# Kernel tuning notes

Hardware: AMD Instinct MI355X
Metric: run time of the kernel (lower is better)

Reference implementation:

```python
import jax, jax.numpy as jnp
import numpy as np

N_NODES = 100000
N_EDGES = 1600000
IN_DIM = 64
OUT_DIM = 64


def setup_inputs() -> dict:
    key = jax.random.key(0)
    k_x, k_e, k_wm, k_bm, k_wu, k_bu = jax.random.split(key, 6)
    x = jax.random.normal(k_x, (N_NODES, IN_DIM), dtype=jnp.float32)
    edge_index = jax.random.randint(k_e, (2, N_EDGES), 0, N_NODES, dtype=jnp.int64)
    # PyTorch Linear default init: U(-1/sqrt(fan_in), 1/sqrt(fan_in))
    lim_m = 1.0 / np.sqrt(2 * IN_DIM)
    lim_u = 1.0 / np.sqrt(IN_DIM + OUT_DIM)
    W_msg = jax.random.uniform(k_wm, (2 * IN_DIM, OUT_DIM), jnp.float32, -lim_m, lim_m)
    b_msg = jax.random.uniform(k_bm, (OUT_DIM,), jnp.float32, -lim_m, lim_m)
    W_upd = jax.random.uniform(k_wu, (IN_DIM + OUT_DIM, OUT_DIM), jnp.float32, -lim_u, lim_u)
    b_upd = jax.random.uniform(k_bu, (OUT_DIM,), jnp.float32, -lim_u, lim_u)
    return {"x": x, "edge_index": edge_index, "W_msg": W_msg, "b_msg": b_msg,
            "W_upd": W_upd, "b_upd": b_upd}


def reference(x, edge_index, W_msg, b_msg, W_upd, b_upd):
    num_nodes = x.shape[0]
    source, target = edge_index[0], edge_index[1]
    # gather endpoint features and compute messages: [E, 2*in] -> [E, out]
    edge_feats = jnp.concatenate([x[source], x[target]], axis=-1)
    messages = jax.nn.relu(edge_feats @ W_msg + b_msg)
    # mean aggregation onto target nodes
    agg_sum = jax.ops.segment_sum(messages, target, num_segments=num_nodes)
    counts = jax.ops.segment_sum(jnp.ones_like(target, dtype=x.dtype), target,
                                 num_segments=num_nodes)
    aggregated = agg_sum / jnp.clip(counts, 1.0, None)[:, None]
    # update MLP: [N, in+out] -> [N, out]
    updated = jax.nn.relu(jnp.concatenate([x, aggregated], axis=-1) @ W_upd + b_upd)
    return updated
```

## Files before the change

kernel.cpp:

```cpp
#include <hip/hip_runtime.h>
#include <hip/hip_bf16.h>

#define N_NODES 100000
#define N_EDGES 1600000
#define DIM 64
#define NB 196
#define CAP 9216
#define SMASK 0x1FFFFu
#define P1 391
#define T1 781
#define R1 (T1 * 64)
#define T2 196

typedef __attribute__((ext_vector_type(8))) short bf16x8;
typedef __attribute__((ext_vector_type(4))) float f32x4;
typedef __attribute__((ext_vector_type(2))) float f32x2;

__device__ __forceinline__ unsigned short f2bs(float f) {
    __hip_bfloat16 h = __float2bfloat16(f);
    return *reinterpret_cast<unsigned short*>(&h);
}

__device__ __forceinline__ void transform_tile(
    const float* __restrict__ x, const unsigned short* WB,
    const float* __restrict__ b_msg,
    unsigned int* __restrict__ Xs8, unsigned int* __restrict__ Xt8,
    int r0, int lane)
{
    f32x4 acc[8];
    #pragma unroll
    for (int ct = 0; ct < 8; ++ct) acc[ct] = (f32x4){0.f, 0.f, 0.f, 0.f};

    const int r = r0 + (lane & 15);
    #pragma unroll
    for (int kk = 0; kk < 2; ++kk) {
        const int off = kk * 32 + ((lane >> 4) << 3);
        const float4* xp = reinterpret_cast<const float4*>(&x[r * 64 + off]);
        const float4 p0 = xp[0], p1 = xp[1];
        bf16x8 a;
        a[0] = (short)f2bs(p0.x); a[1] = (short)f2bs(p0.y);
        a[2] = (short)f2bs(p0.z); a[3] = (short)f2bs(p0.w);
        a[4] = (short)f2bs(p1.x); a[5] = (short)f2bs(p1.y);
        a[6] = (short)f2bs(p1.z); a[7] = (short)f2bs(p1.w);
        #pragma unroll
        for (int ct = 0; ct < 8; ++ct) {
            const bf16x8 b = *reinterpret_cast<const bf16x8*>(
                &WB[(((ct << 1) | kk) * 64 + lane) << 3]);
            acc[ct] = __builtin_amdgcn_mfma_f32_16x16x32_bf16(a, b, acc[ct], 0, 0, 0);
        }
    }

    const int fr = lane & 15;
    const int rb = r0 + ((lane >> 4) << 2);
    const float bj0 = b_msg[fr],      bj1 = b_msg[16 + fr];
    const float bj2 = b_msg[32 + fr], bj3 = b_msg[48 + fr];
    #pragma unroll
    for (int q = 0; q < 4; ++q) {
        unsigned int xs = 0;
        xs = (unsigned)__builtin_amdgcn_cvt_pk_fp8_f32(acc[0][q], acc[1][q], (int)xs, false);
        xs = (unsigned)__builtin_amdgcn_cvt_pk_fp8_f32(acc[2][q], acc[3][q], (int)xs, true);
        Xs8[(rb + q) * 16 + fr] = xs;
        unsigned int xt = 0;
        xt = (unsigned)__builtin_amdgcn_cvt_pk_fp8_f32(acc[4][q] + bj0, acc[5][q] + bj1, (int)xt, false);
        xt = (unsigned)__builtin_amdgcn_cvt_pk_fp8_f32(acc[6][q] + bj2, acc[7][q] + bj3, (int)xt, true);
        Xt8[(rb + q) * 16 + fr] = xt;
    }
}

__global__ __launch_bounds__(256) void k1_part_xform(
    const float* __restrict__ x, const float* __restrict__ W_msg,
    const float* __restrict__ b_msg,
    unsigned int* __restrict__ Xs8, unsigned int* __restrict__ Xt8,
    const int* __restrict__ eidx, int* __restrict__ bcursor,
    unsigned int* __restrict__ pairs,
    const float* __restrict__ W_upd, unsigned short* __restrict__ wfrag)
{
    __shared__ __align__(16) char smem[35200];
    const int tid = threadIdx.x, lane = tid & 63, wid = tid >> 6;

    if (blockIdx.x >= P1 + T1) {
        for (int i = tid; i < 8192; i += 256) {
            const int j = i & 7, l = (i >> 3) & 63, kk = (i >> 9) & 3, ct = i >> 11;
            const int hi = l >> 4;
            int k;
            if (kk < 2) k = kk * 32 + (hi << 3) + j;
            else        k = 64 + ((j & 3) << 4) + ((kk - 2) << 3) + (hi << 1) + (j >> 2);
            const int c = ct * 16 + (l & 15);
            wfrag[i] = f2bs(W_upd[k * 64 + c]);
        }
    } else if (blockIdx.x >= P1) {
        unsigned short* WB = reinterpret_cast<unsigned short*>(smem);
        const int tb = blockIdx.x - P1;
        for (int i = tid; i < 8192; i += 256) {
            const int j = i & 7, l = (i >> 3) & 63, kk = (i >> 9) & 1, ct = i >> 10;
            const int k = kk * 32 + ((l >> 4) << 3) + j;
            const int c = ct * 16 + (l & 15);
            WB[i] = f2bs(W_msg[(((c >> 6) << 6) + k) * 64 + (c & 63)]);
        }
        __syncthreads();
        transform_tile(x, WB, b_msg, Xs8, Xt8, tb * 64 + wid * 16, lane);
    } else {
        unsigned int* sbuf = reinterpret_cast<unsigned int*>(smem);
        int* dbase = reinterpret_cast<int*>(smem + 16384);
        int* tcnt  = reinterpret_cast<int*>(smem + 32768);
        int* toff  = tcnt + NB;
        int* gpos  = toff + NB;
        int* wsum  = gpos + NB;

        const int base = blockIdx.x * 4096;
        const int tcount = min(4096, N_EDGES - base);
        if (tid < NB) tcnt[tid] = 0;
        __syncthreads();

        unsigned int pk[16]; int bb[16]; int rk[16];
        #pragma unroll
        for (int j = 0; j < 16; ++j) {
            const int idx = base + j * 256 + tid;
            bb[j] = -1;
            if (idx < N_EDGES) {
                const int sv = eidx[idx];
                const int tv = eidx[N_EDGES + idx];
                bb[j] = tv >> 9;
                pk[j] = (unsigned)sv | ((unsigned)(tv & 511) << 17);
                rk[j] = atomicAdd(&tcnt[bb[j]], 1);
            }
        }
        __syncthreads();

        const int v = (tid < NB) ? tcnt[tid] : 0;
        int s = v;
        #pragma unroll
        for (int d = 1; d < 64; d <<= 1) { int u = __shfl_up(s, d); if (lane >= d) s += u; }
        if (lane == 63) wsum[wid] = s;
        __syncthreads();
        if (wid == 0) {
            int ws = (lane < 4) ? wsum[lane] : 0;
            #pragma unroll
            for (int d = 1; d < 4; d <<= 1) { int u = __shfl_up(ws, d); if (lane >= d) ws += u; }
            if (lane < 4) wsum[lane] = ws;
        }
        __syncthreads();
        const int exc = (wid ? wsum[wid - 1] : 0) + s - v;
        if (tid < NB) {
            toff[tid] = exc;
            gpos[tid] = tid * CAP + (v ? atomicAdd(&bcursor[tid], v) : 0);
        }
        __syncthreads();

        #pragma unroll
        for (int j = 0; j < 16; ++j) {
            if (bb[j] >= 0) {
                const int l = toff[bb[j]] + rk[j];
                sbuf[l]  = pk[j];
                dbase[l] = gpos[bb[j]] + rk[j];
            }
        }
        __syncthreads();
        for (int i = tid; i < tcount; i += 256)
            pairs[dbase[i]] = sbuf[i];
    }
}

__global__ __launch_bounds__(1024) void k2_sort_xform(
    const int* __restrict__ bcursor, const unsigned int* __restrict__ pairs,
    int* __restrict__ csr, int* __restrict__ deg, int* __restrict__ row,
    const float* __restrict__ x, const float* __restrict__ W_msg,
    const float* __restrict__ b_msg,
    unsigned int* __restrict__ Xs8, unsigned int* __restrict__ Xt8)
{
    __shared__ __align__(16) char smem[59424];
    const int tid = threadIdx.x, lane = tid & 63, wid = tid >> 6;

    if (blockIdx.x >= NB) {
        unsigned short* WB = reinterpret_cast<unsigned short*>(smem);
        const int tb = blockIdx.x - NB;
        for (int i = tid; i < 8192; i += 1024) {
            const int j = i & 7, l = (i >> 3) & 63, kk = (i >> 9) & 1, ct = i >> 10;
            const int k = kk * 32 + ((l >> 4) << 3) + j;
            const int c = ct * 16 + (l & 15);
            WB[i] = f2bs(W_msg[(((c >> 6) << 6) + k) * 64 + (c & 63)]);
        }
        __syncthreads();
        const int r0 = R1 + tb * 256 + wid * 16;
        if (r0 >= N_NODES) return;
        transform_tile(x, WB, b_msg, Xs8, Xt8, r0, lane);
    } else {
        unsigned int*   ebuf = reinterpret_cast<unsigned int*>(smem);
        unsigned short* rbuf = reinterpret_cast<unsigned short*>(smem + 36864);
        int* ncnt = reinterpret_cast<int*>(smem + 55296);
        int* noff = reinterpret_cast<int*>(smem + 57344);
        int* wsum = reinterpret_cast<int*>(smem + 59392);

        const int b = blockIdx.x;
        const int s0 = b * CAP;
        const int cnt = bcursor[b];
        if (tid < 512) ncnt[tid] = 0;
        __syncthreads();

        for (int i = tid; i < cnt; i += 1024) {
            const unsigned int p = pairs[s0 + i];
            ebuf[i] = p;
            rbuf[i] = (unsigned short)atomicAdd(&ncnt[p >> 17], 1);
        }
        __syncthreads();

        int v = 0, s = 0;
        if (tid < 512) {
            v = ncnt[tid];
            s = v;
            #pragma unroll
            for (int d = 1; d < 64; d <<= 1) { int u = __shfl_up(s, d); if (lane >= d) s += u; }
            if (lane == 63) wsum[wid] = s;
        }
        __syncthreads();
        if (wid == 0) {
            int ws = (lane < 8) ? wsum[lane] : 0;
            #pragma unroll
            for (int d = 1; d < 8; d <<= 1) { int u = __shfl_up(ws, d); if (lane >= d) ws += u; }
            if (lane < 8) wsum[lane] = ws;
        }
        __syncthreads();
        if (tid < 512) {
            const int exc = (wid ? wsum[wid - 1] : 0) + s - v;
            noff[tid] = exc;
            const int n = b * 512 + tid;
            if (n < N_NODES) { deg[n] = v; row[n] = s0 + exc; }
        }
        __syncthreads();

        for (int i = tid; i < cnt; i += 1024) {
            const unsigned int p = ebuf[i];
            csr[s0 + noff[p >> 17] + (int)rbuf[i]] = (int)(p & SMASK);
        }
    }
}

__device__ __forceinline__ void acc_fp8(unsigned int u,
    float t0, float t1, float t2, float t3,
    float& a0, float& a1, float& a2, float& a3)
{
    const f32x2 lo = __builtin_amdgcn_cvt_pk_f32_fp8(u, false);
    const f32x2 hi = __builtin_amdgcn_cvt_pk_f32_fp8(u, true);
    a0 += fmaxf(lo.x + t0, 0.f);
    a1 += fmaxf(lo.y + t1, 0.f);
    a2 += fmaxf(hi.x + t2, 0.f);
    a3 += fmaxf(hi.y + t3, 0.f);
}

__global__ __launch_bounds__(1024, 8) void agg_update(
    const int* __restrict__ row, const int* __restrict__ deg,
    const int* __restrict__ csr,
    const unsigned int* __restrict__ Xs8, const unsigned int* __restrict__ Xt8,
    const float* __restrict__ x, const unsigned short* __restrict__ wfrag,
    const float* __restrict__ b_upd, float* __restrict__ out)
{
    __shared__ unsigned short WB[8192];
    __shared__ uint2 aggT[16][18];

    const int tid = threadIdx.x, lane = tid & 63, w = tid >> 6;
    const int n0 = blockIdx.x * 16;
    const int fr = lane & 15, hi = lane >> 4;

    float4 px0, px1, px2, px3; float bj = 0.f;
    if (w < 4) {
        const int r = n0 + fr;
        const float4* xp = reinterpret_cast<const float4*>(&x[r * 64 + (hi << 3)]);
        px0 = xp[0]; px1 = xp[1];
        const float4* xq = reinterpret_cast<const float4*>(&x[r * 64 + 32 + (hi << 3)]);
        px2 = xq[0]; px3 = xq[1];
        bj = b_upd[w * 16 + fr];
    }

    reinterpret_cast<bf16x8*>(WB)[tid] = reinterpret_cast<const bf16x8*>(wfrag)[tid];

    const int n = n0 + w;
    const int c = lane & 15, q = lane >> 4;
    const int start = row[n], d = deg[n];
    const unsigned int tp = Xt8[n * 16 + c];
    const f32x2 tlo = __builtin_amdgcn_cvt_pk_f32_fp8(tp, false);
    const f32x2 thi = __builtin_amdgcn_cvt_pk_f32_fp8(tp, true);
    const float t0 = tlo.x, t1 = tlo.y, t2 = thi.x, t3 = thi.y;
    float a0 = 0.f, a1 = 0.f, a2 = 0.f, a3 = 0.f;

    if (d > 0) {
        int i = 0;
        for (; i + 32 <= d; i += 32) {
            int sv[8];
            #pragma unroll
            for (int k = 0; k < 8; ++k) sv[k] = csr[start + i + 4 * k + q];
            unsigned int u[8];
            #pragma unroll
            for (int k = 0; k < 8; ++k) u[k] = Xs8[sv[k] * 16 + c];
            #pragma unroll
            for (int k = 0; k < 8; ++k) acc_fp8(u[k], t0, t1, t2, t3, a0, a1, a2, a3);
        }
        const int rem = d - i;
        if (rem > 0) {
            const int lastIdx = start + d - 1;
            int sv[8]; bool vm[8];
            #pragma unroll
            for (int k = 0; k < 8; ++k) {
                const int e = i + 4 * k + q;
                vm[k] = (e < d);
                sv[k] = csr[vm[k] ? (start + e) : lastIdx];
            }
            unsigned int u[8];
            #pragma unroll
            for (int k = 0; k < 8; ++k) u[k] = Xs8[sv[k] * 16 + c];
            #pragma unroll
            for (int k = 0; k < 8; ++k) {
                const f32x2 lo = __builtin_amdgcn_cvt_pk_f32_fp8(u[k], false);
                const f32x2 hi2 = __builtin_amdgcn_cvt_pk_f32_fp8(u[k], true);
                if (vm[k]) {
                    a0 += fmaxf(lo.x + t0, 0.f);
                    a1 += fmaxf(lo.y + t1, 0.f);
                    a2 += fmaxf(hi2.x + t2, 0.f);
                    a3 += fmaxf(hi2.y + t3, 0.f);
                }
            }
        }
    }

    a0 += __shfl_xor(a0, 16); a0 += __shfl_xor(a0, 32);
    a1 += __shfl_xor(a1, 16); a1 += __shfl_xor(a1, 32);
    a2 += __shfl_xor(a2, 16); a2 += __shfl_xor(a2, 32);
    a3 += __shfl_xor(a3, 16); a3 += __shfl_xor(a3, 32);
    if (q == 0) {
        const float inv = (d > 0) ? 1.0f / (float)d : 0.f;
        uint2 v2;
        v2.x = (unsigned)f2bs(a0 * inv) | ((unsigned)f2bs(a1 * inv) << 16);
        v2.y = (unsigned)f2bs(a2 * inv) | ((unsigned)f2bs(a3 * inv) << 16);
        aggT[w][c] = v2;
    }
    __syncthreads();

    if (w < 4) {
        const int ct = w;
        f32x4 acc = (f32x4){0.f, 0.f, 0.f, 0.f};
        #pragma unroll
        for (int kk = 0; kk < 4; ++kk) {
            bf16x8 a;
            if (kk == 0) {
                a[0] = (short)f2bs(px0.x); a[1] = (short)f2bs(px0.y);
                a[2] = (short)f2bs(px0.z); a[3] = (short)f2bs(px0.w);
                a[4] = (short)f2bs(px1.x); a[5] = (short)f2bs(px1.y);
                a[6] = (short)f2bs(px1.z); a[7] = (short)f2bs(px1.w);
            } else if (kk == 1) {
                a[0] = (short)f2bs(px2.x); a[1] = (short)f2bs(px2.y);
                a[2] = (short)f2bs(px2.z); a[3] = (short)f2bs(px2.w);
                a[4] = (short)f2bs(px3.x); a[5] = (short)f2bs(px3.y);
                a[6] = (short)f2bs(px3.z); a[7] = (short)f2bs(px3.w);
            } else {
                a = *reinterpret_cast<const bf16x8*>(
                    &aggT[fr][((kk - 2) << 3) + (hi << 1)]);
            }
            const bf16x8 b = *reinterpret_cast<const bf16x8*>(
                &WB[(((ct << 2) | kk) * 64 + lane) << 3]);
            acc = __builtin_amdgcn_mfma_f32_16x16x32_bf16(a, b, acc, 0, 0, 0);
        }
        const int rb = n0 + (hi << 2);
        const int cc = ct * 16 + fr;
        #pragma unroll
        for (int qq = 0; qq < 4; ++qq)
            out[(rb + qq) * 64 + cc] = fmaxf(acc[qq] + bj, 0.f);
    }
}

extern "C" void kernel_launch(void* const* d_in, const int* in_sizes, int n_in,
                              void* d_out, int out_size, void* d_ws, size_t ws_size,
                              hipStream_t stream) {
    const float* x     = (const float*)d_in[0];
    const int*   eidx  = (const int*)  d_in[1];
    const float* W_msg = (const float*)d_in[2];
    const float* b_msg = (const float*)d_in[3];
    const float* W_upd = (const float*)d_in[4];
    const float* b_upd = (const float*)d_in[5];
    float* out = (float*)d_out;

    int* deg     = (int*)d_ws;
    int* row     = deg + N_NODES;
    int* bcursor = row + N_NODES;
    unsigned short* wfrag = (unsigned short*)(bcursor + 256);
    unsigned int* pairs = (unsigned int*)(wfrag + 8192);
    int* csr     = (int*)(pairs + NB * CAP);
    unsigned int* Xs8 = (unsigned int*)(csr + NB * CAP);
    unsigned int* Xt8 = Xs8 + (size_t)N_NODES * 16;

    hipMemsetAsync(bcursor, 0, NB * sizeof(int), stream);
    k1_part_xform<<<P1 + T1 + 1, 256, 0, stream>>>(
        x, W_msg, b_msg, Xs8, Xt8, eidx, bcursor, pairs, W_upd, wfrag);
    k2_sort_xform<<<NB + T2, 1024, 0, stream>>>(
        bcursor, pairs, csr, deg, row, x, W_msg, b_msg, Xs8, Xt8);
    agg_update<<<N_NODES / 16, 1024, 0, stream>>>(row, deg, csr, Xs8, Xt8,
                                                  x, wfrag, b_upd, out);
}
```

Measured before the change: 102.1 us.

## Split neighbor gather by source-index half to improve cache locality of Xs8

The CSR build now sorts each node's edges by whether the source index falls below or above 50000 and records the split point per node. Aggregation runs as two passes: a new kernel sums the low-half sources into a bf16 partial buffer, then the fused update kernel sums the high-half sources, adds the partial, and applies the MLP. The aim is to keep each pass's working set of the FP8 source table small enough to stay cache-resident and to reduce random-gather misses. Streaming loads are switched to nontemporal hints. The cost is an extra kernel launch, a partial-sum round trip through memory, and bf16 rounding of the partial sum.

```diff
diff --git a/kernel.cpp b/kernel.cpp
--- a/kernel.cpp
+++ b/kernel.cpp
@@ -7,6 +7,7 @@
 #define NB 196
 #define CAP 9216
 #define SMASK 0x1FFFFu
+#define HALF_SRC 50000
 #define P1 391
 #define T1 781
 #define R1 (T1 * 64)
@@ -15,11 +16,17 @@
 typedef __attribute__((ext_vector_type(8))) short bf16x8;
 typedef __attribute__((ext_vector_type(4))) float f32x4;
 typedef __attribute__((ext_vector_type(2))) float f32x2;
+typedef __attribute__((ext_vector_type(2))) unsigned int u32x2;
 
 __device__ __forceinline__ unsigned short f2bs(float f) {
     __hip_bfloat16 h = __float2bfloat16(f);
     return *reinterpret_cast<unsigned short*>(&h);
 }
+__device__ __forceinline__ float bs2f(unsigned int u16) {
+    return __uint_as_float(u16 << 16);
+}
+template <typename T>
+__device__ __forceinline__ T ntload(const T* p) { return __builtin_nontemporal_load(p); }
 
 __device__ __forceinline__ void transform_tile(
     const float* __restrict__ x, const unsigned short* WB,
@@ -164,11 +171,12 @@
 __global__ __launch_bounds__(1024) void k2_sort_xform(
     const int* __restrict__ bcursor, const unsigned int* __restrict__ pairs,
     int* __restrict__ csr, int* __restrict__ deg, int* __restrict__ row,
+    int* __restrict__ mid,
     const float* __restrict__ x, const float* __restrict__ W_msg,
     const float* __restrict__ b_msg,
     unsigned int* __restrict__ Xs8, unsigned int* __restrict__ Xt8)
 {
-    __shared__ __align__(16) char smem[59424];
+    __shared__ __align__(16) char smem[63616];
     const int tid = threadIdx.x, lane = tid & 63, wid = tid >> 6;
 
     if (blockIdx.x >= NB) {
@@ -188,49 +196,52 @@
         unsigned int*   ebuf = reinterpret_cast<unsigned int*>(smem);
         unsigned short* rbuf = reinterpret_cast<unsigned short*>(smem + 36864);
         int* ncnt = reinterpret_cast<int*>(smem + 55296);
-        int* noff = reinterpret_cast<int*>(smem + 57344);
-        int* wsum = reinterpret_cast<int*>(smem + 59392);
+        int* noff = reinterpret_cast<int*>(smem + 59392);
+        int* wsum = reinterpret_cast<int*>(smem + 63488);
 
         const int b = blockIdx.x;
         const int s0 = b * CAP;
         const int cnt = bcursor[b];
-        if (tid < 512) ncnt[tid] = 0;
+        ncnt[tid] = 0;
         __syncthreads();
 
         for (int i = tid; i < cnt; i += 1024) {
             const unsigned int p = pairs[s0 + i];
+            const int key = (int)((p >> 17) << 1) | ((p & SMASK) >= HALF_SRC ? 1 : 0);
             ebuf[i] = p;
-            rbuf[i] = (unsigned short)atomicAdd(&ncnt[p >> 17], 1);
-        }
-        __syncthreads();
-
-        int v = 0, s = 0;
+            rbuf[i] = (unsigned short)atomicAdd(&ncnt[key], 1);
+        }
+        __syncthreads();
+
+        const int v = ncnt[tid];
+        int s = v;
+        #pragma unroll
+        for (int d = 1; d < 64; d <<= 1) { int u = __shfl_up(s, d); if (lane >= d) s += u; }
+        if (lane == 63) wsum[wid] = s;
+        __syncthreads();
+        if (wid == 0) {
+            int ws = (lane < 16) ? wsum[lane] : 0;
+            #pragma unroll
+            for (int d = 1; d < 16; d <<= 1) { int u = __shfl_up(ws, d); if (lane >= d) ws += u; }
+            if (lane < 16) wsum[lane] = ws;
+        }
+        __syncthreads();
+        const int exc = (wid ? wsum[wid - 1] : 0) + s - v;
+        noff[tid] = exc;
+        __syncthreads();
+
         if (tid < 512) {
-            v = ncnt[tid];
-            s = v;
-            #pragma unroll
-            for (int d = 1; d < 64; d <<= 1) { int u = __shfl_up(s, d); if (lane >= d) s += u; }
-            if (lane == 63) wsum[wid] = s;
-        }
-        __syncthreads();
-        if (wid == 0) {
-            int ws = (lane < 8) ? wsum[lane] : 0;
-            #pragma unroll
-            for (int d = 1; d < 8; d <<= 1) { int u = __shfl_up(ws, d); if (lane >= d) ws += u; }
-            if (lane < 8) wsum[lane] = ws;
-        }
-        __syncthreads();
-        if (tid < 512) {
-            const int exc = (wid ? wsum[wid - 1] : 0) + s - v;
-            noff[tid] = exc;
             const int n = b * 512 + tid;
-            if (n < N_NODES) { deg[n] = v; row[n] = s0 + exc; }
-        }
-        __syncthreads();
-
+            if (n < N_NODES) {
+                deg[n] = ncnt[2 * tid] + ncnt[2 * tid + 1];
+                mid[n] = ncnt[2 * tid];
+                row[n] = s0 + noff[2 * tid];
+            }
+        }
         for (int i = tid; i < cnt; i += 1024) {
             const unsigned int p = ebuf[i];
-            csr[s0 + noff[p >> 17] + (int)rbuf[i]] = (int)(p & SMASK);
+            const int key = (int)((p >> 17) << 1) | ((p & SMASK) >= HALF_SRC ? 1 : 0);
+            csr[s0 + noff[key] + (int)rbuf[i]] = (int)(p & SMASK);
         }
     }
 }
@@ -247,85 +258,132 @@
     a3 += fmaxf(hi.y + t3, 0.f);
 }
 
-__global__ __launch_bounds__(1024, 8) void agg_update(
-    const int* __restrict__ row, const int* __restrict__ deg,
+__device__ __forceinline__ void gather_range(
+    const int* __restrict__ csr, const unsigned int* __restrict__ Xs8,
+    int start, int cnt2, int c, int q,
+    float t0, float t1, float t2, float t3,
+    float& a0, float& a1, float& a2, float& a3)
+{
+    if (cnt2 <= 0) return;
+    int i = 0;
+    for (; i + 32 <= cnt2; i += 32) {
+        int sv[8];
+        #pragma unroll
+        for (int k = 0; k < 8; ++k) sv[k] = ntload(&csr[start + i + 4 * k + q]);
+        unsigned int u[8];
+        #pragma unroll
+        for (int k = 0; k < 8; ++k) u[k] = Xs8[sv[k] * 16 + c];
+        #pragma unroll
+        for (int k = 0; k < 8; ++k) acc_fp8(u[k], t0, t1, t2, t3, a0, a1, a2, a3);
+    }
+    const int rem = cnt2 - i;
+    if (rem > 0) {
+        const int lastIdx = start + cnt2 - 1;
+        int sv[8]; bool vm[8];
+        #pragma unroll
+        for (int k = 0; k < 8; ++k) {
+            const int e = i + 4 * k + q;
+            vm[k] = (e < cnt2);
+            sv[k] = ntload(&csr[vm[k] ? (start + e) : lastIdx]);
+        }
+        unsigned int u[8];
+        #pragma unroll
+        for (int k = 0; k < 8; ++k) u[k] = Xs8[sv[k] * 16 + c];
+        #pragma unroll
+        for (int k = 0; k < 8; ++k) {
+            const f32x2 lo = __builtin_amdgcn_cvt_pk_f32_fp8(u[k], false);
+            const f32x2 hi = __builtin_amdgcn_cvt_pk_f32_fp8(u[k], true);
+            if (vm[k]) {
+                a0 += fmaxf(lo.x + t0, 0.f);
+                a1 += fmaxf(lo.y + t1, 0.f);
+                a2 += fmaxf(hi.x + t2, 0.f);
+                a3 += fmaxf(hi.y + t3, 0.f);
+            }
+        }
+    }
+}
+
+__global__ __launch_bounds__(256) void aggregate_half(
+    const int* __restrict__ row, const int* __restrict__ mid,
     const int* __restrict__ csr,
     const unsigned int* __restrict__ Xs8, const unsigned int* __restrict__ Xt8,
-    const float* __restrict__ x, const unsigned short* __restrict__ wfrag,
-    const float* __restrict__ b_upd, float* __restrict__ out)
-{
-    __shared__ unsigned short WB[8192];
-    __shared__ uint2 aggT[16][18];
-
-    const int tid = threadIdx.x, lane = tid & 63, w = tid >> 6;
-    const int n0 = blockIdx.x * 16;
-    const int fr = lane & 15, hi = lane >> 4;
-
-    float4 px0, px1, px2, px3; float bj = 0.f;
-    if (w < 4) {
-        const int r = n0 + fr;
-        const float4* xp = reinterpret_cast<const float4*>(&x[r * 64 + (hi << 3)]);
-        px0 = xp[0]; px1 = xp[1];
-        const float4* xq = reinterpret_cast<const float4*>(&x[r * 64 + 32 + (hi << 3)]);
-        px2 = xq[0]; px3 = xq[1];
-        bj = b_upd[w * 16 + fr];
-    }
-
-    reinterpret_cast<bf16x8*>(WB)[tid] = reinterpret_cast<const bf16x8*>(wfrag)[tid];
-
-    const int n = n0 + w;
+    u32x2* __restrict__ aggP)
+{
+    const int n = blockIdx.x * 4 + (threadIdx.x >> 6);
+    const int lane = threadIdx.x & 63;
+    if (n >= N_NODES) return;
     const int c = lane & 15, q = lane >> 4;
-    const int start = row[n], d = deg[n];
-    const unsigned int tp = Xt8[n * 16 + c];
+    const int start = ntload(&row[n]);
+    const int m = ntload(&mid[n]);
+    const unsigned int tp = ntload(&Xt8[n * 16 + c]);
     const f32x2 tlo = __builtin_amdgcn_cvt_pk_f32_fp8(tp, false);
     const f32x2 thi = __builtin_amdgcn_cvt_pk_f32_fp8(tp, true);
-    const float t0 = tlo.x, t1 = tlo.y, t2 = thi.x, t3 = thi.y;
     float a0 = 0.f, a1 = 0.f, a2 = 0.f, a3 = 0.f;
 
-    if (d > 0) {
-        int i = 0;
-        for (; i + 32 <= d; i += 32) {
-            int sv[8];
-            #pragma unroll
-            for (int k = 0; k < 8; ++k) sv[k] = csr[start + i + 4 * k + q];
-            unsigned int u[8];
-            #pragma unroll
-            for (int k = 0; k < 8; ++k) u[k] = Xs8[sv[k] * 16 + c];
-            #pragma unroll
-            for (int k = 0; k < 8; ++k) acc_fp8(u[k], t0, t1, t2, t3, a0, a1, a2, a3);
-        }
-        const int rem = d - i;
-        if (rem > 0) {
-            const int lastIdx = start + d - 1;
-            int sv[8]; bool vm[8];
-            #pragma unroll
-            for (int k = 0; k < 8; ++k) {
-                const int e = i + 4 * k + q;
-                vm[k] = (e < d);
-                sv[k] = csr[vm[k] ? (start + e) : lastIdx];
-            }
-            unsigned int u[8];
-            #pragma unroll
-            for (int k = 0; k < 8; ++k) u[k] = Xs8[sv[k] * 16 + c];
-            #pragma unroll
-            for (int k = 0; k < 8; ++k) {
-                const f32x2 lo = __builtin_amdgcn_cvt_pk_f32_fp8(u[k], false);
-                const f32x2 hi2 = __builtin_amdgcn_cvt_pk_f32_fp8(u[k], true);
-                if (vm[k]) {
-                    a0 += fmaxf(lo.x + t0, 0.f);
-                    a1 += fmaxf(lo.y + t1, 0.f);
-                    a2 += fmaxf(hi2.x + t2, 0.f);
-                    a3 += fmaxf(hi2.y + t3, 0.f);
-                }
-            }
-        }
-    }
+    gather_range(csr, Xs8, start, m, c, q, tlo.x, tlo.y, thi.x, thi.y, a0, a1, a2, a3);
 
     a0 += __shfl_xor(a0, 16); a0 += __shfl_xor(a0, 32);
     a1 += __shfl_xor(a1, 16); a1 += __shfl_xor(a1, 32);
     a2 += __shfl_xor(a2, 16); a2 += __shfl_xor(a2, 32);
     a3 += __shfl_xor(a3, 16); a3 += __shfl_xor(a3, 32);
     if (q == 0) {
+        u32x2 v2;
+        v2[0] = (unsigned)f2bs(a0) | ((unsigned)f2bs(a1) << 16);
+        v2[1] = (unsigned)f2bs(a2) | ((unsigned)f2bs(a3) << 16);
+        aggP[n * 16 + c] = v2;
+    }
+}
+
+__global__ __launch_bounds__(1024, 8) void agg_update(
+    const int* __restrict__ row, const int* __restrict__ mid,
+    const int* __restrict__ deg, const int* __restrict__ csr,
+    const unsigned int* __restrict__ Xs8, const unsigned int* __restrict__ Xt8,
+    const u32x2* __restrict__ aggP,
+    const float* __restrict__ x, const unsigned short* __restrict__ wfrag,
+    const float* __restrict__ b_upd, float* __restrict__ out)
+{
+    __shared__ unsigned short WB[8192];
+    __shared__ uint2 aggT[16][18];
+
+    const int tid = threadIdx.x, lane = tid & 63, w = tid >> 6;
+    const int n0 = blockIdx.x * 16;
+    const int fr = lane & 15, hi = lane >> 4;
+
+    f32x4 px0, px1, px2, px3; float bj = 0.f;
+    if (w < 4) {
+        const int r = n0 + fr;
+        px0 = ntload(reinterpret_cast<const f32x4*>(&x[r * 64 + (hi << 3)]));
+        px1 = ntload(reinterpret_cast<const f32x4*>(&x[r * 64 + (hi << 3) + 4]));
+        px2 = ntload(reinterpret_cast<const f32x4*>(&x[r * 64 + 32 + (hi << 3)]));
+        px3 = ntload(reinterpret_cast<const f32x4*>(&x[r * 64 + 32 + (hi << 3) + 4]));
+        bj = b_upd[w * 16 + fr];
+    }
+
+    reinterpret_cast<bf16x8*>(WB)[tid] = reinterpret_cast<const bf16x8*>(wfrag)[tid];
+
+    const int n = n0 + w;
+    const int c = lane & 15, q = lane >> 4;
+    const int start = ntload(&row[n]);
+    const int m = ntload(&mid[n]);
+    const int d = ntload(&deg[n]);
+    const unsigned int tp = ntload(&Xt8[n * 16 + c]);
+    const f32x2 tlo = __builtin_amdgcn_cvt_pk_f32_fp8(tp, false);
+    const f32x2 thi = __builtin_amdgcn_cvt_pk_f32_fp8(tp, true);
+    float a0 = 0.f, a1 = 0.f, a2 = 0.f, a3 = 0.f;
+
+    gather_range(csr, Xs8, start + m, d - m, c, q, tlo.x, tlo.y, thi.x, thi.y,
+                 a0, a1, a2, a3);
+
+    a0 += __shfl_xor(a0, 16); a0 += __shfl_xor(a0, 32);
+    a1 += __shfl_xor(a1, 16); a1 += __shfl_xor(a1, 32);
+    a2 += __shfl_xor(a2, 16); a2 += __shfl_xor(a2, 32);
+    a3 += __shfl_xor(a3, 16); a3 += __shfl_xor(a3, 32);
+    if (q == 0) {
+        const u32x2 par = ntload(&aggP[n * 16 + c]);
+        a0 += bs2f(par[0] & 0xffffu);
+        a1 += bs2f(par[0] >> 16);
+        a2 += bs2f(par[1] & 0xffffu);
+        a3 += bs2f(par[1] >> 16);
         const float inv = (d > 0) ? 1.0f / (float)d : 0.f;
         uint2 v2;
         v2.x = (unsigned)f2bs(a0 * inv) | ((unsigned)f2bs(a1 * inv) << 16);
@@ -341,15 +399,15 @@
         for (int kk = 0; kk < 4; ++kk) {
             bf16x8 a;
             if (kk == 0) {
-                a[0] = (short)f2bs(px0.x); a[1] = (short)f2bs(px0.y);
-                a[2] = (short)f2bs(px0.z); a[3] = (short)f2bs(px0.w);
-                a[4] = (short)f2bs(px1.x); a[5] = (short)f2bs(px1.y);
-                a[6] = (short)f2bs(px1.z); a[7] = (short)f2bs(px1.w);
+                a[0] = (short)f2bs(px0[0]); a[1] = (short)f2bs(px0[1]);
+                a[2] = (short)f2bs(px0[2]); a[3] = (short)f2bs(px0[3]);
+                a[4] = (short)f2bs(px1[0]); a[5] = (short)f2bs(px1[1]);
+                a[6] = (short)f2bs(px1[2]); a[7] = (short)f2bs(px1[3]);
             } else if (kk == 1) {
-                a[0] = (short)f2bs(px2.x); a[1] = (short)f2bs(px2.y);
-                a[2] = (short)f2bs(px2.z); a[3] = (short)f2bs(px2.w);
-                a[4] = (short)f2bs(px3.x); a[5] = (short)f2bs(px3.y);
-                a[6] = (short)f2bs(px3.z); a[7] = (short)f2bs(px3.w);
+                a[0] = (short)f2bs(px2[0]); a[1] = (short)f2bs(px2[1]);
+                a[2] = (short)f2bs(px2[2]); a[3] = (short)f2bs(px2[3]);
+                a[4] = (short)f2bs(px3[0]); a[5] = (short)f2bs(px3[1]);
+                a[6] = (short)f2bs(px3[2]); a[7] = (short)f2bs(px3[3]);
             } else {
                 a = *reinterpret_cast<const bf16x8*>(
                     &aggT[fr][((kk - 2) << 3) + (hi << 1)]);
@@ -379,18 +437,22 @@
 
     int* deg     = (int*)d_ws;
     int* row     = deg + N_NODES;
-    int* bcursor = row + N_NODES;
+    int* mid     = row + N_NODES;
+    int* bcursor = mid + N_NODES;
     unsigned short* wfrag = (unsigned short*)(bcursor + 256);
     unsigned int* pairs = (unsigned int*)(wfrag + 8192);
     int* csr     = (int*)(pairs + NB * CAP);
     unsigned int* Xs8 = (unsigned int*)(csr + NB * CAP);
     unsigned int* Xt8 = Xs8 + (size_t)N_NODES * 16;
+    u32x2* aggP  = (u32x2*)(Xt8 + (size_t)N_NODES * 16);
 
     hipMemsetAsync(bcursor, 0, NB * sizeof(int), stream);
     k1_part_xform<<<P1 + T1 + 1, 256, 0, stream>>>(
         x, W_msg, b_msg, Xs8, Xt8, eidx, bcursor, pairs, W_upd, wfrag);
     k2_sort_xform<<<NB + T2, 1024, 0, stream>>>(
-        bcursor, pairs, csr, deg, row, x, W_msg, b_msg, Xs8, Xt8);
-    agg_update<<<N_NODES / 16, 1024, 0, stream>>>(row, deg, csr, Xs8, Xt8,
-                                                  x, wfrag, b_upd, out);
-}
+        bcursor, pairs, csr, deg, row, mid, x, W_msg, b_msg, Xs8, Xt8);
+    aggregate_half<<<(N_NODES + 3) / 4, 256, 0, stream>>>(
+        row, mid, csr, Xs8, Xt8, aggP);
+    agg_update<<<N_NODES / 16, 1024, 0, stream>>>(
+        row, mid, deg, csr, Xs8, Xt8, aggP, x, wfrag, b_upd, out);
+}
```

Result: slower. 159.1 us (+55.8%).
